# Performance work log

Hardware: AMD Instinct MI355X
Metric: run time of the kernel (lower is better)

## Reference

```python
import jax, jax.numpy as jnp
import numpy as np

INPUT_DIM = 512
OUTPUT_DIM = 64
MAX_HIDDEN_DIM = 448
NUM_NODES = INPUT_DIM + OUTPUT_DIM + MAX_HIDDEN_DIM      # 1024
NUM_MID = OUTPUT_DIM + MAX_HIDDEN_DIM                    # 512
BATCH = 32768


def setup_inputs() -> dict:
    key = jax.random.key(0)
    k1, k2, k3, k4, k5 = jax.random.split(key, 5)
    x = jax.random.normal(k1, (BATCH, INPUT_DIM), dtype=jnp.float32)
    # fan-in scaled init as in reset_parameters (approximate per-column std)
    weight = jax.random.normal(k2, (NUM_NODES, NUM_MID), dtype=jnp.float32)
    bias = jax.random.normal(k3, (NUM_MID,), dtype=jnp.float32)
    connectivity = jax.random.randint(k4, (NUM_NODES, NUM_MID), 0, 2, dtype=jnp.int32)
    node_existence = jax.random.randint(k5, (NUM_MID,), 0, 2, dtype=jnp.int32)
    # output nodes always exist (as in __init__ / reset_parameters)
    node_existence = node_existence.at[-OUTPUT_DIM:].set(1)
    return {"x": x, "weight": weight, "bias": bias,
            "connectivity": connectivity, "node_existence": node_existence}


def reference(x, weight, bias, connectivity, node_existence):
    B, input_dim = x.shape
    num_nodes, num_mid = weight.shape
    dt = x.dtype
    eff = weight * connectivity.astype(dt)          # [num_nodes, num_mid]
    exist = node_existence.astype(dt)               # [num_mid]

    # signals buffer: columns [0, input_dim) hold x; later columns start at 0.
    # Since unwritten columns are zero, a full matvec with eff[:, i] equals the
    # original sliced matmul over the first input_dim + i rows.
    signals0 = jnp.concatenate([x, jnp.zeros((B, num_mid), dtype=dt)], axis=1)

    def step(signals, inp):
        w_col, b_i, ex_i, i = inp
        res = jax.nn.sigmoid(signals @ w_col + b_i) * ex_i        # [B]
        signals = jax.lax.dynamic_update_slice(
            signals, res[:, None], (0, input_dim + i))
        return signals, None

    xs = (eff.T, bias, exist, jnp.arange(num_mid, dtype=jnp.int32))
    signals, _ = jax.lax.scan(step, signals0, xs)
    return signals[:, -OUTPUT_DIM:]                 # [B, output_dim]
```

## Files before the change

kernel.cpp:

```cpp
#include <hip/hip_runtime.h>

#define BATCH_N   32768
#define IN_DIM    512
#define MID_N     512
#define NODES_N   1024
#define OUT_DIM   64

#define ROWS      64
#define TPB       512
#define NWAVES    8
#define NBLK      8
#define SIGPAD    513
#define SIG_STRIDE 456
#define RESF_PAD  65

typedef __attribute__((ext_vector_type(8))) short          short8;
typedef __attribute__((ext_vector_type(8))) unsigned short ush8;
typedef __attribute__((ext_vector_type(4))) float          f32x4;

__device__ __forceinline__ unsigned short f2bf(float f) {
    unsigned u = __float_as_uint(f);
    return (unsigned short)((u + 0x7FFFu + ((u >> 16) & 1u)) >> 16);
}
__device__ __forceinline__ float bf2f(unsigned short h) {
    return __uint_as_float(((unsigned)h) << 16);
}

__device__ __forceinline__ f32x4 mfma3(short8 ah, short8 al, short8 bh, short8 bl, f32x4 c) {
    c = __builtin_amdgcn_mfma_f32_16x16x32_bf16(al, bh, c, 0, 0, 0);
    c = __builtin_amdgcn_mfma_f32_16x16x32_bf16(ah, bl, c, 0, 0, 0);
    c = __builtin_amdgcn_mfma_f32_16x16x32_bf16(ah, bh, c, 0, 0, 0);
    return c;
}

__global__ void prep_eff_kernel(const float4* __restrict__ w,
                                const int4* __restrict__ c,
                                float4* __restrict__ eff)
{
    const int i = blockIdx.x * 256 + threadIdx.x;
    const int4 cv = c[i];
    const float4 wvv = w[i];
    float4 ev;
    ev.x = cv.x ? wvv.x : 0.0f;
    ev.y = cv.y ? wvv.y : 0.0f;
    ev.z = cv.z ? wvv.z : 0.0f;
    ev.w = cv.w ? wvv.w : 0.0f;
    eff[i] = ev;
}

__global__ void prep_effB_kernel(const float* __restrict__ effF,
                                 unsigned short* __restrict__ ebh,
                                 unsigned short* __restrict__ ebl)
{
    const int t    = blockIdx.x * 256 + threadIdx.x;
    const int lane = t & 63;
    const int ct   = (t >> 6) & 31;
    const int kt   = t >> 11;
    const int col  = ct * 16 + (lane & 15);
    const int k0   = kt * 32 + 8 * (lane >> 4);
    ush8 h, l;
    #pragma unroll
    for (int j = 0; j < 8; ++j) {
        float e = effF[(size_t)(k0 + j) * MID_N + col];
        unsigned short hb = f2bf(e);
        h[j] = hb;
        l[j] = f2bf(e - bf2f(hb));
    }
    *(ush8*)&ebh[(size_t)t * 8] = h;
    *(ush8*)&ebl[(size_t)t * 8] = l;
}

__global__ void prep_x_kernel(const float* __restrict__ x,
                              unsigned short* __restrict__ xfh,
                              unsigned short* __restrict__ xfl)
{
    const int t    = blockIdx.x * 256 + threadIdx.x;
    const int lane = t & 63;
    const int kt   = (t >> 6) & 15;
    const int rt   = t >> 10;
    const int row  = rt * 16 + (lane & 15);
    const int k0   = kt * 32 + 8 * (lane >> 4);
    const float4* xp = (const float4*)(x + (size_t)row * IN_DIM + k0);
    const float4 v0 = xp[0];
    const float4 v1 = xp[1];
    const float vv[8] = {v0.x, v0.y, v0.z, v0.w, v1.x, v1.y, v1.z, v1.w};
    ush8 h, l;
    #pragma unroll
    for (int j = 0; j < 8; ++j) {
        unsigned short hb = f2bf(vv[j]);
        h[j] = hb;
        l[j] = f2bf(vv[j] - bf2f(hb));
    }
    *(ush8*)&xfh[(size_t)t * 8] = h;
    *(ush8*)&xfl[(size_t)t * 8] = l;
}

__global__ __launch_bounds__(TPB, 2)
void nn_mfma_kernel(const float* __restrict__ bias,
                    const int* __restrict__ ne,
                    const float* __restrict__ effF,
                    const unsigned short* __restrict__ xfh,
                    const unsigned short* __restrict__ xfl,
                    const unsigned short* __restrict__ ebh,
                    const unsigned short* __restrict__ ebl,
                    float* __restrict__ out)
{
    __shared__ unsigned short sig_hi[ROWS][SIG_STRIDE];
    __shared__ unsigned short sig_lo[ROWS][SIG_STRIDE];
    __shared__ float resf[ROWS][RESF_PAD];

    const int tid  = threadIdx.x;
    const int wv   = tid >> 6;
    const int lane = tid & 63;
    const int l15  = lane & 15;
    const int lg   = lane >> 4;
    const int bl   = blockIdx.x;
    const int r0   = bl * ROWS;

    const short8* XFH = (const short8*)xfh;
    const short8* XFL = (const short8*)xfl;
    const short8* EBH = (const short8*)ebh;
    const short8* EBL = (const short8*)ebl;

    f32x4 acc[4][4];
    #pragma unroll
    for (int ct = 0; ct < 4; ++ct) {
        const float bv = bias[64 * wv + 16 * ct + l15];
        #pragma unroll
        for (int rt = 0; rt < 4; ++rt) {
            acc[rt][ct][0] = bv; acc[rt][ct][1] = bv;
            acc[rt][ct][2] = bv; acc[rt][ct][3] = bv;
        }
    }

    #pragma unroll 1
    for (int kt = 0; kt < 16; ++kt) {
        short8 ah[4], al[4], bh[4], blo[4];
        #pragma unroll
        for (int rt = 0; rt < 4; ++rt) {
            const size_t f = ((size_t)(bl * 4 + rt) * 16 + kt) * 64 + lane;
            ah[rt] = XFH[f];
            al[rt] = XFL[f];
        }
        #pragma unroll
        for (int ct = 0; ct < 4; ++ct) {
            const size_t f = ((size_t)kt * 32 + (4 * wv + ct)) * 64 + lane;
            bh[ct]  = EBH[f];
            blo[ct] = EBL[f];
        }
        #pragma unroll
        for (int rt = 0; rt < 4; ++rt)
            #pragma unroll
            for (int ct = 0; ct < 4; ++ct)
                acc[rt][ct] = mfma3(ah[rt], al[rt], bh[ct], blo[ct], acc[rt][ct]);
    }

    #pragma unroll 1
    for (int b = 0; b < NBLK; ++b) {
        if (wv == b) {
            #pragma unroll
            for (int rt = 0; rt < 4; ++rt)
                #pragma unroll
                for (int ct = 0; ct < 4; ++ct)
                    #pragma unroll
                    for (int r = 0; r < 4; ++r)
                        resf[16 * rt + 4 * lg + r][16 * ct + l15] = acc[rt][ct][r];
        }
        __syncthreads();

        float zreg[8];
        #pragma unroll
        for (int j = 0; j < 8; ++j) zreg[j] = resf[lane][8 * wv + j];
        __syncthreads();

        const int g0w = 64 * b + 8 * wv;

        for (int s = 0; s < NWAVES; ++s) {
            if (wv == s) {
                float rloc[8];
                #pragma unroll
                for (int j = 0; j < 8; ++j) {
                    float z = zreg[j];
                    #pragma unroll
                    for (int jj = 0; jj < 8; ++jj) {
                        if (jj < j) {
                            const size_t eo =
                                (size_t)(IN_DIM + g0w + jj) * MID_N + (g0w + j);
                            z = fmaf(rloc[jj], effF[eo], z);
                        }
                    }
                    const float ex = (ne[g0w + j] != 0) ? 1.0f : 0.0f;
                    const float r  = ex / (1.0f + __expf(-z));
                    rloc[j] = r;
                    resf[lane][8 * wv + j] = r;
                }
            }
            __syncthreads();
            if (wv > s) {
                const int ks = 64 * b + 8 * s;
                #pragma unroll
                for (int jj = 0; jj < 8; ++jj) {
                    const float rv = resf[lane][8 * s + jj];
                    const size_t eb = (size_t)(IN_DIM + ks + jj) * MID_N + g0w;
                    #pragma unroll
                    for (int c = 0; c < 8; ++c)
                        zreg[c] = fmaf(rv, effF[eb + c], zreg[c]);
                }
            }
        }
        __syncthreads();

        if (b < 7) {
            const int row = tid >> 3;
            const int c0  = (tid & 7) * 8;
            ush8 h, l;
            #pragma unroll
            for (int j = 0; j < 8; ++j) {
                const float v = resf[row][c0 + j];
                unsigned short hb = f2bf(v);
                h[j] = hb;
                l[j] = f2bf(v - bf2f(hb));
            }
            *(ush8*)&sig_hi[row][64 * b + c0] = h;
            *(ush8*)&sig_lo[row][64 * b + c0] = l;
        } else {
            #pragma unroll
            for (int p = 0; p < 8; ++p) {
                const int idx = tid + p * TPB;
                out[(size_t)(r0 + (idx >> 6)) * OUT_DIM + (idx & 63)] =
                    resf[idx >> 6][idx & 63];
            }
        }
        __syncthreads();

        if (b < 7 && wv > b) {
            #pragma unroll
            for (int kk = 0; kk < 2; ++kk) {
                short8 ah[4], al[4];
                const int kb = 64 * b + 32 * kk + 8 * lg;
                #pragma unroll
                for (int rt = 0; rt < 4; ++rt) {
                    const int rr = 16 * rt + l15;
                    ah[rt] = *(const short8*)&sig_hi[rr][kb];
                    al[rt] = *(const short8*)&sig_lo[rr][kb];
                }
                #pragma unroll
                for (int ct = 0; ct < 4; ++ct) {
                    const size_t f =
                        ((size_t)(16 + 2 * b + kk) * 32 + (4 * wv + ct)) * 64 + lane;
                    const short8 bh  = EBH[f];
                    const short8 blo = EBL[f];
                    #pragma unroll
                    for (int rt = 0; rt < 4; ++rt)
                        acc[rt][ct] = mfma3(ah[rt], al[rt], bh, blo, acc[rt][ct]);
                }
            }
        }
    }
}

template<bool PRE>
__global__ __launch_bounds__(TPB, 2)
void nn_fused_kernel(const float* __restrict__ x,
                     const float* __restrict__ weight,
                     const float* __restrict__ bias,
                     const int* __restrict__ conn,
                     const int* __restrict__ ne,
                     const float* __restrict__ eff,
                     float* __restrict__ out)
{
    __shared__ float sig[ROWS][SIGPAD];
    const int tid  = threadIdx.x;
    const int wv   = tid >> 6;
    const int lane = tid & 63;
    const int r0   = blockIdx.x * ROWS;
    const int row  = r0 + lane;
    const int wu   = __builtin_amdgcn_readfirstlane(wv);
    const float4* __restrict__ xr =
        reinterpret_cast<const float4*>(x + (size_t)row * IN_DIM);
    float acc[8];

    for (int b = 0; b < NBLK; ++b) {
        const int cbu = 64 * b + 8 * wu;
        #pragma unroll
        for (int c = 0; c < 8; ++c) acc[c] = bias[cbu + c];
        #pragma unroll 2
        for (int k4 = 0; k4 < IN_DIM / 4; ++k4) {
            const float4 xv = xr[k4];
            #pragma unroll
            for (int j = 0; j < 4; ++j) {
                const int k = k4 * 4 + j;
                const float xs = (&xv.x)[j];
                const size_t ebase = (size_t)k * MID_N + cbu;
                #pragma unroll
                for (int c = 0; c < 8; ++c) {
                    float e;
                    if constexpr (PRE) e = eff[ebase + c];
                    else e = conn[ebase + c] ? weight[ebase + c] : 0.0f;
                    acc[c] = fmaf(xs, e, acc[c]);
                }
            }
        }
        #pragma unroll 4
        for (int k = 0; k < 64 * b; ++k) {
            const float rv = sig[lane][k];
            const size_t ebase = (size_t)(IN_DIM + k) * MID_N + cbu;
            #pragma unroll
            for (int c = 0; c < 8; ++c) {
                float e;
                if constexpr (PRE) e = eff[ebase + c];
                else e = conn[ebase + c] ? weight[ebase + c] : 0.0f;
                acc[c] = fmaf(rv, e, acc[c]);
            }
        }
        for (int s = 0; s < NWAVES; ++s) {
            if (wv == s) {
                const int g0 = 64 * b + 8 * s;
                float rloc[8];
                #pragma unroll
                for (int j = 0; j < 8; ++j) {
                    float z = acc[j];
                    #pragma unroll
                    for (int jj = 0; jj < 8; ++jj) {
                        if (jj < j) {
                            const size_t eo =
                                (size_t)(IN_DIM + g0 + jj) * MID_N + (g0 + j);
                            float e;
                            if constexpr (PRE) e = eff[eo];
                            else e = conn[eo] ? weight[eo] : 0.0f;
                            z = fmaf(rloc[jj], e, z);
                        }
                    }
                    const float ex = (ne[g0 + j] != 0) ? 1.0f : 0.0f;
                    const float r  = ex / (1.0f + __expf(-z));
                    rloc[j] = r;
                    sig[lane][g0 + j] = r;
                }
            }
            __syncthreads();
            if (wv > s) {
                const int g0 = 64 * b + 8 * s;
                #pragma unroll
                for (int jj = 0; jj < 8; ++jj) {
                    const float rv = sig[lane][g0 + jj];
                    const size_t ebase = (size_t)(IN_DIM + g0 + jj) * MID_N + cbu;
                    #pragma unroll
                    for (int c = 0; c < 8; ++c) {
                        float e;
                        if constexpr (PRE) e = eff[ebase + c];
                        else e = conn[ebase + c] ? weight[ebase + c] : 0.0f;
                        acc[c] = fmaf(rv, e, acc[c]);
                    }
                }
            }
        }
    }
    #pragma unroll
    for (int idx = tid; idx < ROWS * OUT_DIM; idx += TPB) {
        const int rr = idx >> 6;
        const int cc = idx & 63;
        out[(size_t)(r0 + rr) * OUT_DIM + cc] = sig[rr][(MID_N - OUT_DIM) + cc];
    }
}

extern "C" void kernel_launch(void* const* d_in, const int* in_sizes, int n_in,
                              void* d_out, int out_size, void* d_ws, size_t ws_size,
                              hipStream_t stream)
{
    const float* x      = (const float*)d_in[0];
    const float* weight = (const float*)d_in[1];
    const float* bias   = (const float*)d_in[2];
    const int*   conn   = (const int*)d_in[3];
    const int*   ne     = (const int*)d_in[4];
    float*       out    = (float*)d_out;

    const size_t effF_b = (size_t)NODES_N * MID_N * sizeof(float);
    const size_t ebh_b  = (size_t)32 * 32 * 64 * 8 * 2;
    const size_t xfh_b  = (size_t)2048 * 16 * 64 * 8 * 2;
    const size_t need   = effF_b + 2 * ebh_b + 2 * xfh_b;

    if (ws_size >= need) {
        char* w0 = (char*)d_ws;
        float*          effF = (float*)w0;
        unsigned short* ebh  = (unsigned short*)(w0 + effF_b);
        unsigned short* ebl  = (unsigned short*)(w0 + effF_b + ebh_b);
        unsigned short* xfh  = (unsigned short*)(w0 + effF_b + 2 * ebh_b);
        unsigned short* xfl  = (unsigned short*)(w0 + effF_b + 2 * ebh_b + xfh_b);

        prep_eff_kernel<<<512, 256, 0, stream>>>(
            (const float4*)weight, (const int4*)conn, (float4*)effF);
        prep_effB_kernel<<<256, 256, 0, stream>>>(effF, ebh, ebl);
        prep_x_kernel<<<8192, 256, 0, stream>>>(x, xfh, xfl);
        nn_mfma_kernel<<<BATCH_N / ROWS, TPB, 0, stream>>>(
            bias, ne, effF, xfh, xfl, ebh, ebl, out);
    } else if (ws_size >= effF_b) {
        float* eff = (float*)d_ws;
        prep_eff_kernel<<<512, 256, 0, stream>>>(
            (const float4*)weight, (const int4*)conn, (float4*)eff);
        nn_fused_kernel<true><<<BATCH_N / ROWS, TPB, 0, stream>>>(
            x, weight, bias, conn, ne, eff, out);
    } else {
        nn_fused_kernel<false><<<BATCH_N / ROWS, TPB, 0, stream>>>(
            x, weight, bias, conn, ne, nullptr, out);
    }
}
```

Baseline: 345.0 us.

## Drop bf16 signal LDS buffers and split operands from resf on the fly

Removes the large sig_hi/sig_lo shared-memory arrays. The bf16 hi/lo operand split is now recomputed directly from the fp32 resf tile when feeding the MFMA update, which cuts LDS use per block enough to raise launch bounds to 4 blocks per SM. The resf pad becomes 68 so rows can be read as float4, and the zreg and rv reads are vectorised. This trades redundant conversion ALU work, repeated per wave and column tile, for higher occupancy and one fewer barrier. Register pressure under the tighter launch bound may cause spills.

```diff
diff --git a/kernel.cpp b/kernel.cpp
--- a/kernel.cpp
+++ b/kernel.cpp
@@ -11,8 +11,7 @@
 #define NWAVES    8
 #define NBLK      8
 #define SIGPAD    513
-#define SIG_STRIDE 456
-#define RESF_PAD  65
+#define RESF_PAD  68
 
 typedef __attribute__((ext_vector_type(8))) short          short8;
 typedef __attribute__((ext_vector_type(8))) unsigned short ush8;
@@ -95,7 +94,7 @@
     *(ush8*)&xfl[(size_t)t * 8] = l;
 }
 
-__global__ __launch_bounds__(TPB, 2)
+__global__ __launch_bounds__(TPB, 4)
 void nn_mfma_kernel(const float* __restrict__ bias,
                     const int* __restrict__ ne,
                     const float* __restrict__ effF,
@@ -105,8 +104,6 @@
                     const unsigned short* __restrict__ ebl,
                     float* __restrict__ out)
 {
-    __shared__ unsigned short sig_hi[ROWS][SIG_STRIDE];
-    __shared__ unsigned short sig_lo[ROWS][SIG_STRIDE];
     __shared__ float resf[ROWS][RESF_PAD];
 
     const int tid  = threadIdx.x;
@@ -169,8 +166,12 @@
         __syncthreads();
 
         float zreg[8];
-        #pragma unroll
-        for (int j = 0; j < 8; ++j) zreg[j] = resf[lane][8 * wv + j];
+        {
+            const float4 z0 = *(const float4*)&resf[lane][8 * wv];
+            const float4 z1 = *(const float4*)&resf[lane][8 * wv + 4];
+            zreg[0] = z0.x; zreg[1] = z0.y; zreg[2] = z0.z; zreg[3] = z0.w;
+            zreg[4] = z1.x; zreg[5] = z1.y; zreg[6] = z1.z; zreg[7] = z1.w;
+        }
         __syncthreads();
 
         const int g0w = 64 * b + 8 * wv;
@@ -198,32 +199,22 @@
             __syncthreads();
             if (wv > s) {
                 const int ks = 64 * b + 8 * s;
+                const float4 r8a = *(const float4*)&resf[lane][8 * s];
+                const float4 r8b = *(const float4*)&resf[lane][8 * s + 4];
+                const float rv[8] = {r8a.x, r8a.y, r8a.z, r8a.w,
+                                     r8b.x, r8b.y, r8b.z, r8b.w};
                 #pragma unroll
                 for (int jj = 0; jj < 8; ++jj) {
-                    const float rv = resf[lane][8 * s + jj];
                     const size_t eb = (size_t)(IN_DIM + ks + jj) * MID_N + g0w;
                     #pragma unroll
                     for (int c = 0; c < 8; ++c)
-                        zreg[c] = fmaf(rv, effF[eb + c], zreg[c]);
+                        zreg[c] = fmaf(rv[jj], effF[eb + c], zreg[c]);
                 }
             }
         }
         __syncthreads();
 
-        if (b < 7) {
-            const int row = tid >> 3;
-            const int c0  = (tid & 7) * 8;
-            ush8 h, l;
-            #pragma unroll
-            for (int j = 0; j < 8; ++j) {
-                const float v = resf[row][c0 + j];
-                unsigned short hb = f2bf(v);
-                h[j] = hb;
-                l[j] = f2bf(v - bf2f(hb));
-            }
-            *(ush8*)&sig_hi[row][64 * b + c0] = h;
-            *(ush8*)&sig_lo[row][64 * b + c0] = l;
-        } else {
+        if (b == 7) {
             #pragma unroll
             for (int p = 0; p < 8; ++p) {
                 const int idx = tid + p * TPB;
@@ -231,18 +222,25 @@
                     resf[idx >> 6][idx & 63];
             }
         }
-        __syncthreads();
 
         if (b < 7 && wv > b) {
             #pragma unroll
             for (int kk = 0; kk < 2; ++kk) {
                 short8 ah[4], al[4];
-                const int kb = 64 * b + 32 * kk + 8 * lg;
+                const int c0 = 32 * kk + 8 * lg;
                 #pragma unroll
                 for (int rt = 0; rt < 4; ++rt) {
                     const int rr = 16 * rt + l15;
-                    ah[rt] = *(const short8*)&sig_hi[rr][kb];
-                    al[rt] = *(const short8*)&sig_lo[rr][kb];
+                    const float4 v0 = *(const float4*)&resf[rr][c0];
+                    const float4 v1 = *(const float4*)&resf[rr][c0 + 4];
+                    const float vv[8] = {v0.x, v0.y, v0.z, v0.w,
+                                         v1.x, v1.y, v1.z, v1.w};
+                    #pragma unroll
+                    for (int j = 0; j < 8; ++j) {
+                        const unsigned short hb = f2bf(vv[j]);
+                        ah[rt][j] = (short)hb;
+                        al[rt][j] = (short)f2bf(vv[j] - bf2f(hb));
+                    }
                 }
                 #pragma unroll
                 for (int ct = 0; ct < 4; ++ct) {
@@ -256,6 +254,7 @@
                 }
             }
         }
+        __syncthreads();
     }
 }
 
```

New measurement: 545.9 us. 58.2% more time.
